# Kernel optimization log

Hardware: AMD Instinct MI355X
Metric: run time of the kernel (lower is better)

## Reference

```python
import jax, jax.numpy as jnp
import numpy as np

B, S, D, E = 4, 4096, 1024, 8
TOP_K = 2


def setup_inputs() -> dict:
    key = jax.random.key(0)
    k_x, k_gw, k_gb, k_ew, k_eb = jax.random.split(key, 5)
    x = jax.random.normal(k_x, (B, S, D), dtype=jnp.float32)
    gate_w = jax.random.normal(k_gw, (E, D), dtype=jnp.float32) * 0.02
    gate_b = jax.random.normal(k_gb, (E,), dtype=jnp.float32) * 0.02
    expert_w = jax.random.normal(k_ew, (E, D, D), dtype=jnp.float32) * 0.02
    expert_b = jax.random.normal(k_eb, (E, D), dtype=jnp.float32) * 0.02
    return {"x": x, "gate_w": gate_w, "gate_b": gate_b,
            "expert_w": expert_w, "expert_b": expert_b}


def reference(x, gate_w, gate_b, expert_w, expert_b):
    b, s, d = x.shape
    h = x.reshape(-1, d)                                  # [T, D]
    # router: linear -> softmax (fp32) -> top-k -> renormalize
    router_logits = h @ gate_w.T + gate_b                 # [T, E]
    probs = jax.nn.softmax(router_logits.astype(jnp.float32), axis=-1)
    topw, sel = jax.lax.top_k(probs, TOP_K)               # [T, K]
    topw = topw / jnp.sum(topw, axis=-1, keepdims=True)
    topw = topw.astype(h.dtype)
    out = jnp.zeros_like(h)
    for e in range(E):  # small fixed loop over experts
        # per-token combine weight for expert e (0 if not selected)
        we = jnp.sum(jnp.where(sel == e, topw, 0.0), axis=-1)  # [T]
        out = out + (h @ expert_w[e].T + expert_b[e]) * we[:, None]
    return out.reshape(b, s, d), router_logits
```

## Files before the change

kernel.cpp:

```cpp
#include <hip/hip_runtime.h>
#include <hip/hip_bf16.h>

typedef unsigned short u16;
typedef unsigned int u32;

#define T_TOK 16384
#define DIM   1024
#define NEXP  8

#define XB_OFF      0
#define WB_OFF      33554432
#define CNT_OFF     50331648
#define LIST_OFF    50332160
#define SELW_OFF    50856448
#define CONTRIB_OFF 51380736
#define WS_NEED     118489600ULL

__device__ __forceinline__ u16 f2bf(float f) {
    u32 u = __float_as_uint(f);
    u += 0x7fff + ((u >> 16) & 1);
    return (u16)(u >> 16);
}
__device__ __forceinline__ float bf2f(u16 u) {
    return __uint_as_float(((u32)u) << 16);
}

#define RT_PB 32

__global__ __launch_bounds__(256) void k_router(
    const float* __restrict__ x, const float* __restrict__ gw,
    const float* __restrict__ gb, float* __restrict__ logits,
    u16* __restrict__ xb, int* __restrict__ counts,
    int* __restrict__ lists, float4* __restrict__ selw,
    const float* __restrict__ ew, u16* __restrict__ wb)
{
    const int tid  = threadIdx.x;
    const int lane = tid & 63;
    const int w    = tid >> 6;

    __shared__ int   s_sel0[RT_PB], s_sel1[RT_PB];
    __shared__ int   s_lcnt[NEXP], s_gbase[NEXP];

    if (tid < NEXP) s_lcnt[tid] = 0;

    for (int i = 0; i < 8; ++i) {
        const int l = w * 8 + i;
        const int t = blockIdx.x * RT_PB + l;

        const float* xr = x + (size_t)t * DIM;
        float4 xs[4];
#pragma unroll
        for (int j = 0; j < 4; ++j)
            xs[j] = *reinterpret_cast<const float4*>(xr + (j * 64 + lane) * 4);

        float acc[NEXP];
#pragma unroll
        for (int e = 0; e < NEXP; ++e) {
            const float* gr = gw + e * DIM;
            float s = 0.f;
#pragma unroll
            for (int j = 0; j < 4; ++j) {
                float4 g = *reinterpret_cast<const float4*>(gr + (j * 64 + lane) * 4);
                s += xs[j].x * g.x + xs[j].y * g.y + xs[j].z * g.z + xs[j].w * g.w;
            }
            acc[e] = s;
        }
#pragma unroll
        for (int off = 1; off < 64; off <<= 1) {
#pragma unroll
            for (int e = 0; e < NEXP; ++e) acc[e] += __shfl_xor(acc[e], off);
        }
#pragma unroll
        for (int e = 0; e < NEXP; ++e) acc[e] += gb[e];

        int i0 = 0; float v0 = acc[0];
#pragma unroll
        for (int e = 1; e < NEXP; ++e) if (acc[e] > v0) { v0 = acc[e]; i0 = e; }
        int i1 = -1; float v1 = -3.4e38f;
#pragma unroll
        for (int e = 0; e < NEXP; ++e) if (e != i0 && acc[e] > v1) { v1 = acc[e]; i1 = e; }
        float e1  = __expf(v1 - v0);
        float inv = 1.f / (1.f + e1);
        float w0 = inv, w1 = e1 * inv;

        u16* xrow = xb + (size_t)t * DIM;
#pragma unroll
        for (int j = 0; j < 4; ++j) {
            int c = (j * 64 + lane) * 4;
            float4 v = xs[j];
            ushort4 u;
            u.x = f2bf(v.x); u.y = f2bf(v.y); u.z = f2bf(v.z); u.w = f2bf(v.w);
            *reinterpret_cast<ushort4*>(xrow + c) = u;
        }
        if (lane == 0) {
            float4 lo = make_float4(acc[0], acc[1], acc[2], acc[3]);
            float4 hi = make_float4(acc[4], acc[5], acc[6], acc[7]);
            *reinterpret_cast<float4*>(logits + (size_t)t * NEXP)     = lo;
            *reinterpret_cast<float4*>(logits + (size_t)t * NEXP + 4) = hi;
            selw[t] = make_float4(__int_as_float(i0), __int_as_float(i1), w0, w1);
            s_sel0[l] = i0; s_sel1[l] = i1;
        }
    }
    __syncthreads();

    int i0 = 0, i1 = 0, r0 = 0, r1 = 0;
    if (tid < RT_PB) {
        i0 = s_sel0[tid]; i1 = s_sel1[tid];
        r0 = atomicAdd(&s_lcnt[i0], 1);
        r1 = atomicAdd(&s_lcnt[i1], 1);
    }
    __syncthreads();
    if (tid < NEXP)
        s_gbase[tid] = atomicAdd(&counts[tid * 16], s_lcnt[tid]);
    __syncthreads();
    if (tid < RT_PB) {
        int t  = blockIdx.x * RT_PB + tid;
        lists[i0 * T_TOK + s_gbase[i0] + r0] = t * 2;
        lists[i1 * T_TOK + s_gbase[i1] + r1] = t * 2 + 1;
    }

    const int n4 = NEXP * DIM * DIM / 4;
    const int stride = gridDim.x * 256;
    for (int i = blockIdx.x * 256 + tid; i < n4; i += stride) {
        float4 v = reinterpret_cast<const float4*>(ew)[i];
        ushort4 u;
        u.x = f2bf(v.x); u.y = f2bf(v.y); u.z = f2bf(v.z); u.w = f2bf(v.w);
        reinterpret_cast<ushort4*>(wb)[i] = u;
    }
}


typedef __attribute__((ext_vector_type(8))) short bf16x8;
typedef __attribute__((ext_vector_type(4))) float f32x4;

#define GLDS16(g, l) __builtin_amdgcn_global_load_lds( \
    (const __attribute__((address_space(1))) void*)(g), \
    (__attribute__((address_space(3))) void*)(l), 16, 0, 0)

#define BAR() __builtin_amdgcn_s_barrier()
#define PRIO1() __builtin_amdgcn_s_setprio(1)
#define PRIO0() __builtin_amdgcn_s_setprio(0)
#define VMW0() asm volatile("s_waitcnt vmcnt(0)" ::: "memory")
#define LGKM0() do { asm volatile("s_waitcnt lgkmcnt(0)" ::: "memory"); \
                     __builtin_amdgcn_sched_barrier(0); } while (0)

__global__ __launch_bounds__(256, 2) void k_gemm(
    const u16* __restrict__ xb, const u16* __restrict__ wb,
    const int* __restrict__ counts, const int* __restrict__ lists,
    u16* __restrict__ contrib)
{
    __shared__ char lds[65536];

    const int bid = (blockIdx.x & 7) * 1024 + (blockIdx.x >> 3);
    const int e   = bid >> 10;
    const int mt  = (bid >> 3) & 127;
    const int nt  = bid & 7;
    const int cnt = counts[e * 16];
    if (mt * 128 >= cnt) return;

    const int tid  = threadIdx.x;
    const int lane = tid & 63;
    const int wid  = tid >> 6;
    const int wm   = wid >> 1;
    const int wn   = wid & 1;
    const int listbase = e * T_TOK;

    const int l8  = lane >> 3;
    const int cgs = ((lane & 7) - l8) & 7;
    const char* xbB = (const char*)xb;
    const char* wbB = (const char*)wb;
    u32 aoff[4], boff[4];
#pragma unroll
    for (int i = 0; i < 4; ++i) {
        int r    = wid * 32 + i * 8 + l8;
        int slot = mt * 128 + r;
        int tok  = lists[listbase + (slot < cnt ? slot : cnt - 1)] >> 1;
        aoff[i]  = (u32)tok * 2048 + (u32)cgs * 16;
        boff[i]  = ((u32)e << 21) + (u32)(nt * 128 + r) * 2048 + (u32)cgs * 16;
    }

#define STAGE(b, t) do { \
    _Pragma("unroll") for (int i = 0; i < 4; ++i) \
        GLDS16(xbB + aoff[i] + (t) * 128, lds + (b) * 32768 + (wid * 4 + i) * 1024); \
    _Pragma("unroll") for (int i = 0; i < 4; ++i) \
        GLDS16(wbB + boff[i] + (t) * 128, lds + (b) * 32768 + 16384 + (wid * 4 + i) * 1024); \
} while (0)

    const int l15 = lane & 15;
    const int c0  = lane >> 4;
    const u32 ra0 = (u32)(wm * 64 + l15) * 128 + (u32)(((c0 + l15) & 7) * 16);
    const u32 ra1 = (u32)(wm * 64 + l15) * 128 + (u32)(((4 + c0 + l15) & 7) * 16);
    const u32 rb0 = 16384u + (u32)(wn * 64 + l15) * 128 + (u32)(((c0 + l15) & 7) * 16);
    const u32 rb1 = 16384u + (u32)(wn * 64 + l15) * 128 + (u32)(((4 + c0 + l15) & 7) * 16);

    bf16x8 A0[8], B0[8], A1[8], B1[8];
#define LDSET(Ad, Bd, b) do { \
    _Pragma("unroll") for (int mi = 0; mi < 4; ++mi) { \
        Ad[mi * 2 + 0] = *(const bf16x8*)(lds + (b) * 32768 + ra0 + mi * 2048); \
        Ad[mi * 2 + 1] = *(const bf16x8*)(lds + (b) * 32768 + ra1 + mi * 2048); \
    } \
    _Pragma("unroll") for (int ni = 0; ni < 4; ++ni) { \
        Bd[ni * 2 + 0] = *(const bf16x8*)(lds + (b) * 32768 + rb0 + ni * 2048); \
        Bd[ni * 2 + 1] = *(const bf16x8*)(lds + (b) * 32768 + rb1 + ni * 2048); \
    } \
} while (0)

    f32x4 acc[4][4];
#pragma unroll
    for (int mi = 0; mi < 4; ++mi)
#pragma unroll
        for (int ni = 0; ni < 4; ++ni) acc[mi][ni] = (f32x4)0.f;

#define MFMAS(As, Bs) do { \
    _Pragma("unroll") for (int kk = 0; kk < 2; ++kk) \
    _Pragma("unroll") for (int mi = 0; mi < 4; ++mi) \
    _Pragma("unroll") for (int ni = 0; ni < 4; ++ni) \
        acc[mi][ni] = __builtin_amdgcn_mfma_f32_16x16x32_bf16( \
            As[mi * 2 + kk], Bs[ni * 2 + kk], acc[mi][ni], 0, 0, 0); \
} while (0)

#define ITER(U, Ac, Bc, An, Bn) do { \
    LGKM0(); \
    if ((U) >= 1) VMW0(); \
    BAR(); \
    if ((U) <= 13) STAGE((U) & 1, (U) + 2); \
    if ((U) <= 14) LDSET(An, Bn, ((U) + 1) & 1); \
    PRIO1(); MFMAS(Ac, Bc); PRIO0(); \
} while (0)

    STAGE(0, 0); STAGE(1, 1);
    VMW0(); BAR();
    LDSET(A0, B0, 0);

#pragma unroll
    for (int h = 0; h < 8; ++h) {
        ITER(2 * h,     A0, B0, A1, B1);
        ITER(2 * h + 1, A1, B1, A0, B0);
    }

    const int rbase = c0 * 4;
    const int cbase = nt * 128 + wn * 64 + l15;
#pragma unroll
    for (int mi = 0; mi < 4; ++mi) {
#pragma unroll
        for (int r = 0; r < 4; ++r) {
            int slot = mt * 128 + wm * 64 + mi * 16 + rbase + r;
            if (slot < cnt) {
                int lv = lists[listbase + slot];
                u16* crow = contrib + (size_t)lv * DIM + cbase;
#pragma unroll
                for (int ni = 0; ni < 4; ++ni)
                    crow[ni * 16] = f2bf(acc[mi][ni][r]);
            }
        }
    }
}

__global__ __launch_bounds__(256) void k_combine(
    const u16* __restrict__ contrib, const float4* __restrict__ selw,
    const float* __restrict__ eb, float* __restrict__ out)
{
    const int lane = threadIdx.x & 63;
    const int t    = blockIdx.x * 4 + (threadIdx.x >> 6);
    float4 sw = selw[t];
    const int e0 = __float_as_int(sw.x);
    const int e1 = __float_as_int(sw.y);
    const float w0 = sw.z, w1 = sw.w;
    const u16* c0 = contrib + (size_t)(t * 2) * DIM;
    const u16* c1 = c0 + DIM;
    const float* b0 = eb + e0 * DIM;
    const float* b1 = eb + e1 * DIM;
    float* orow = out + (size_t)t * DIM;
#pragma unroll
    for (int j = 0; j < 2; ++j) {
        const int c = (j * 64 + lane) * 8;
        uint4 u0 = *reinterpret_cast<const uint4*>(c0 + c);
        uint4 u1 = *reinterpret_cast<const uint4*>(c1 + c);
        const u16* p0 = (const u16*)&u0;
        const u16* p1 = (const u16*)&u1;
#pragma unroll
        for (int h = 0; h < 2; ++h) {
            float4 bb0 = *reinterpret_cast<const float4*>(b0 + c + h * 4);
            float4 bb1 = *reinterpret_cast<const float4*>(b1 + c + h * 4);
            float4 o;
            o.x = w0 * (bf2f(p0[h*4+0]) + bb0.x) + w1 * (bf2f(p1[h*4+0]) + bb1.x);
            o.y = w0 * (bf2f(p0[h*4+1]) + bb0.y) + w1 * (bf2f(p1[h*4+1]) + bb1.y);
            o.z = w0 * (bf2f(p0[h*4+2]) + bb0.z) + w1 * (bf2f(p1[h*4+2]) + bb1.z);
            o.w = w0 * (bf2f(p0[h*4+3]) + bb0.w) + w1 * (bf2f(p1[h*4+3]) + bb1.w);
            *reinterpret_cast<float4*>(orow + c + h * 4) = o;
        }
    }
}

__global__ __launch_bounds__(256) void k_bias(
    const float4* __restrict__ selw, const float* __restrict__ eb,
    float* __restrict__ out)
{
    const int lane = threadIdx.x & 63;
    const int t    = blockIdx.x * 4 + (threadIdx.x >> 6);
    float4 sw = selw[t];
    const float* b0 = eb + __float_as_int(sw.x) * DIM;
    const float* b1 = eb + __float_as_int(sw.y) * DIM;
    float* orow = out + (size_t)t * DIM;
#pragma unroll
    for (int j = 0; j < 4; ++j) {
        int c = (j * 64 + lane) * 4;
        float4 f0 = *reinterpret_cast<const float4*>(b0 + c);
        float4 f1 = *reinterpret_cast<const float4*>(b1 + c);
        float4 o;
        o.x = sw.z * f0.x + sw.w * f1.x;
        o.y = sw.z * f0.y + sw.w * f1.y;
        o.z = sw.z * f0.z + sw.w * f1.z;
        o.w = sw.z * f0.w + sw.w * f1.w;
        *reinterpret_cast<float4*>(orow + c) = o;
    }
}

__global__ __launch_bounds__(256) void k_gemm_atomic(
    const u16* __restrict__ xb, const u16* __restrict__ wb,
    const int* __restrict__ counts, const int* __restrict__ lists,
    const float4* __restrict__ selw, float* __restrict__ out)
{
    __shared__ u16 ldsA[128 * 64];
    __shared__ u16 ldsB[128 * 64];
    const int bid = blockIdx.x;
    const int e   = bid >> 10;
    const int mt  = (bid >> 3) & 127;
    const int nt  = bid & 7;
    const int cnt = counts[e * 16];
    if (mt * 128 >= cnt) return;
    const int tid  = threadIdx.x;
    const int lane = tid & 63;
    const int wid  = tid >> 6;
    const int wr   = wid >> 1, wc = wid & 1;
    const int srow = tid >> 3;
    const int skc  = (tid & 7) * 8;
    const int listbase = e * T_TOK;
    int tokA[4];
#pragma unroll
    for (int i = 0; i < 4; ++i) {
        int slot = mt * 128 + i * 32 + srow;
        tokA[i] = lists[listbase + (slot < cnt ? slot : cnt - 1)] >> 1;
    }
    const size_t wbase = ((size_t)e << 20) + (size_t)(nt * 128) * DIM;
    f32x4 acc[4][4];
#pragma unroll
    for (int mi = 0; mi < 4; ++mi)
#pragma unroll
        for (int ni = 0; ni < 4; ++ni) acc[mi][ni] = (f32x4)0.f;
    for (int k0 = 0; k0 < DIM; k0 += 64) {
        uint4 ra[4], rb[4];
#pragma unroll
        for (int i = 0; i < 4; ++i) {
            ra[i] = *reinterpret_cast<const uint4*>(xb + (size_t)tokA[i] * DIM + k0 + skc);
            rb[i] = *reinterpret_cast<const uint4*>(wb + wbase + (size_t)(i * 32 + srow) * DIM + k0 + skc);
        }
        __syncthreads();
#pragma unroll
        for (int i = 0; i < 4; ++i) {
            *reinterpret_cast<uint4*>(ldsA + (i * 32 + srow) * 64 + skc) = ra[i];
            *reinterpret_cast<uint4*>(ldsB + (i * 32 + srow) * 64 + skc) = rb[i];
        }
        __syncthreads();
#pragma unroll
        for (int ks = 0; ks < 2; ++ks) {
            const int kof = ks * 32 + (lane >> 4) * 8;
            bf16x8 af[4], bfr[4];
#pragma unroll
            for (int mi = 0; mi < 4; ++mi)
                af[mi] = *reinterpret_cast<const bf16x8*>(ldsA + (wr * 64 + mi * 16 + (lane & 15)) * 64 + kof);
#pragma unroll
            for (int ni = 0; ni < 4; ++ni)
                bfr[ni] = *reinterpret_cast<const bf16x8*>(ldsB + (wc * 64 + ni * 16 + (lane & 15)) * 64 + kof);
#pragma unroll
            for (int mi = 0; mi < 4; ++mi)
#pragma unroll
                for (int ni = 0; ni < 4; ++ni)
                    acc[mi][ni] = __builtin_amdgcn_mfma_f32_16x16x32_bf16(af[mi], bfr[ni], acc[mi][ni], 0, 0, 0);
        }
        __syncthreads();
    }
    const int rbase = (lane >> 4) * 4;
    const int cbase = nt * 128 + wc * 64 + (lane & 15);
#pragma unroll
    for (int mi = 0; mi < 4; ++mi) {
#pragma unroll
        for (int r = 0; r < 4; ++r) {
            int slot = mt * 128 + wr * 64 + mi * 16 + rbase + r;
            if (slot < cnt) {
                int lv = lists[listbase + slot];
                int tok = lv >> 1;
                float4 sw = selw[tok];
                float wgt = (lv & 1) ? sw.w : sw.z;
                float* orow = out + (size_t)tok * DIM + cbase;
#pragma unroll
                for (int ni = 0; ni < 4; ++ni)
                    atomicAdd(orow + ni * 16, acc[mi][ni][r] * wgt);
            }
        }
    }
}

extern "C" void kernel_launch(void* const* d_in, const int* in_sizes, int n_in,
                              void* d_out, int out_size, void* d_ws, size_t ws_size,
                              hipStream_t stream) {
    const float* x  = (const float*)d_in[0];
    const float* gw = (const float*)d_in[1];
    const float* gb = (const float*)d_in[2];
    const float* ew = (const float*)d_in[3];
    const float* eb = (const float*)d_in[4];

    float* out    = (float*)d_out;
    float* logits = out + (size_t)T_TOK * DIM;

    char*   ws      = (char*)d_ws;
    u16*    xb      = (u16*)(ws + XB_OFF);
    u16*    wb      = (u16*)(ws + WB_OFF);
    int*    counts  = (int*)(ws + CNT_OFF);
    int*    lists   = (int*)(ws + LIST_OFF);
    float4* selw    = (float4*)(ws + SELW_OFF);
    u16*    contrib = (u16*)(ws + CONTRIB_OFF);

    hipMemsetAsync((void*)(ws + CNT_OFF), 0, 512, stream);
    k_router<<<T_TOK / RT_PB, 256, 0, stream>>>(x, gw, gb, logits, xb, counts,
                                                lists, selw, ew, wb);

    if (ws_size >= WS_NEED) {
        k_gemm<<<NEXP * 128 * 8, 256, 0, stream>>>(xb, wb, counts, lists, contrib);
        k_combine<<<T_TOK / 4, 256, 0, stream>>>(contrib, selw, eb, out);
    } else {
        k_bias<<<T_TOK / 4, 256, 0, stream>>>(selw, eb, out);
        k_gemm_atomic<<<NEXP * 128 * 8, 256, 0, stream>>>(xb, wb, counts, lists, selw, out);
    }
}
```

Baseline: 154.7 us.

## Enlarge grouped expert GEMM tile to 256x256 with 8 waves and K=32 steps

The expert GEMM moves from 128x128 tiles with 4 waves and a K-step of 64 to 256x256 tiles with 8 waves (512 threads) and a K-step of 32. Each wave now computes a 64x128 sub-tile with 32 accumulators. The LDS swizzle and staging are redone for 64-byte rows, and the grid shrinks accordingly. The aim is more operand reuse per loaded byte and fewer blocks. The costs are higher register pressure (launch bounds 512,2), twice as many barriers per K, and coarser padding waste on the ragged per-expert token counts.

```diff
diff --git a/kernel.cpp b/kernel.cpp
--- a/kernel.cpp
+++ b/kernel.cpp
@@ -144,19 +144,19 @@
 #define LGKM0() do { asm volatile("s_waitcnt lgkmcnt(0)" ::: "memory"); \
                      __builtin_amdgcn_sched_barrier(0); } while (0)
 
-__global__ __launch_bounds__(256, 2) void k_gemm(
+__global__ __launch_bounds__(512, 2) void k_gemm(
     const u16* __restrict__ xb, const u16* __restrict__ wb,
     const int* __restrict__ counts, const int* __restrict__ lists,
     u16* __restrict__ contrib)
 {
     __shared__ char lds[65536];
 
-    const int bid = (blockIdx.x & 7) * 1024 + (blockIdx.x >> 3);
-    const int e   = bid >> 10;
-    const int mt  = (bid >> 3) & 127;
-    const int nt  = bid & 7;
+    const int bid = (blockIdx.x & 7) * 256 + (blockIdx.x >> 3);
+    const int e   = bid >> 8;
+    const int mt  = (bid >> 2) & 63;
+    const int nt  = bid & 3;
     const int cnt = counts[e * 16];
-    if (mt * 128 >= cnt) return;
+    if (mt * 256 >= cnt) return;
 
     const int tid  = threadIdx.x;
     const int lane = tid & 63;
@@ -165,66 +165,59 @@
     const int wn   = wid & 1;
     const int listbase = e * T_TOK;
 
-    const int l8  = lane >> 3;
-    const int cgs = ((lane & 7) - l8) & 7;
+    const int lr  = tid >> 2;
+    const int cgs = (((tid & 3) - lr - (lr >> 2)) & 3);
     const char* xbB = (const char*)xb;
     const char* wbB = (const char*)wb;
-    u32 aoff[4], boff[4];
-#pragma unroll
-    for (int i = 0; i < 4; ++i) {
-        int r    = wid * 32 + i * 8 + l8;
-        int slot = mt * 128 + r;
+    u32 aoff[2], boff[2];
+#pragma unroll
+    for (int i = 0; i < 2; ++i) {
+        int slot = mt * 256 + i * 128 + lr;
         int tok  = lists[listbase + (slot < cnt ? slot : cnt - 1)] >> 1;
         aoff[i]  = (u32)tok * 2048 + (u32)cgs * 16;
-        boff[i]  = ((u32)e << 21) + (u32)(nt * 128 + r) * 2048 + (u32)cgs * 16;
+        boff[i]  = ((u32)e << 21) + (u32)(nt * 256 + i * 128 + lr) * 2048 + (u32)cgs * 16;
     }
 
 #define STAGE(b, t) do { \
-    _Pragma("unroll") for (int i = 0; i < 4; ++i) \
-        GLDS16(xbB + aoff[i] + (t) * 128, lds + (b) * 32768 + (wid * 4 + i) * 1024); \
-    _Pragma("unroll") for (int i = 0; i < 4; ++i) \
-        GLDS16(wbB + boff[i] + (t) * 128, lds + (b) * 32768 + 16384 + (wid * 4 + i) * 1024); \
+    GLDS16(xbB + aoff[0] + (t) * 64, lds + (b) * 32768 + tid * 16); \
+    GLDS16(xbB + aoff[1] + (t) * 64, lds + (b) * 32768 + 8192 + tid * 16); \
+    GLDS16(wbB + boff[0] + (t) * 64, lds + (b) * 32768 + 16384 + tid * 16); \
+    GLDS16(wbB + boff[1] + (t) * 64, lds + (b) * 32768 + 24576 + tid * 16); \
 } while (0)
 
     const int l15 = lane & 15;
     const int c0  = lane >> 4;
-    const u32 ra0 = (u32)(wm * 64 + l15) * 128 + (u32)(((c0 + l15) & 7) * 16);
-    const u32 ra1 = (u32)(wm * 64 + l15) * 128 + (u32)(((4 + c0 + l15) & 7) * 16);
-    const u32 rb0 = 16384u + (u32)(wn * 64 + l15) * 128 + (u32)(((c0 + l15) & 7) * 16);
-    const u32 rb1 = 16384u + (u32)(wn * 64 + l15) * 128 + (u32)(((4 + c0 + l15) & 7) * 16);
-
-    bf16x8 A0[8], B0[8], A1[8], B1[8];
+    const u32 slotw = (u32)(((c0 + l15 + (l15 >> 2)) & 3) * 16);
+    const u32 raB = (u32)(wm * 64 + l15) * 64 + slotw;
+    const u32 rbB = 16384u + (u32)(wn * 128 + l15) * 64 + slotw;
+
+    bf16x8 A0[4], B0[8], A1[4], B1[8];
 #define LDSET(Ad, Bd, b) do { \
-    _Pragma("unroll") for (int mi = 0; mi < 4; ++mi) { \
-        Ad[mi * 2 + 0] = *(const bf16x8*)(lds + (b) * 32768 + ra0 + mi * 2048); \
-        Ad[mi * 2 + 1] = *(const bf16x8*)(lds + (b) * 32768 + ra1 + mi * 2048); \
-    } \
-    _Pragma("unroll") for (int ni = 0; ni < 4; ++ni) { \
-        Bd[ni * 2 + 0] = *(const bf16x8*)(lds + (b) * 32768 + rb0 + ni * 2048); \
-        Bd[ni * 2 + 1] = *(const bf16x8*)(lds + (b) * 32768 + rb1 + ni * 2048); \
-    } \
+    _Pragma("unroll") for (int mi = 0; mi < 4; ++mi) \
+        Ad[mi] = *(const bf16x8*)(lds + (b) * 32768 + raB + mi * 1024); \
+    _Pragma("unroll") for (int ni = 0; ni < 8; ++ni) \
+        Bd[ni] = *(const bf16x8*)(lds + (b) * 32768 + rbB + ni * 1024); \
 } while (0)
 
-    f32x4 acc[4][4];
+    f32x4 acc[4][8];
 #pragma unroll
     for (int mi = 0; mi < 4; ++mi)
 #pragma unroll
-        for (int ni = 0; ni < 4; ++ni) acc[mi][ni] = (f32x4)0.f;
+        for (int ni = 0; ni < 8; ++ni) acc[mi][ni] = (f32x4)0.f;
 
 #define MFMAS(As, Bs) do { \
-    _Pragma("unroll") for (int kk = 0; kk < 2; ++kk) \
     _Pragma("unroll") for (int mi = 0; mi < 4; ++mi) \
-    _Pragma("unroll") for (int ni = 0; ni < 4; ++ni) \
+    _Pragma("unroll") for (int ni = 0; ni < 8; ++ni) \
         acc[mi][ni] = __builtin_amdgcn_mfma_f32_16x16x32_bf16( \
-            As[mi * 2 + kk], Bs[ni * 2 + kk], acc[mi][ni], 0, 0, 0); \
+            As[mi], Bs[ni], acc[mi][ni], 0, 0, 0); \
 } while (0)
 
 #define ITER(U, Ac, Bc, An, Bn) do { \
     LGKM0(); \
     if ((U) >= 1) VMW0(); \
     BAR(); \
-    if ((U) <= 13) STAGE((U) & 1, (U) + 2); \
-    if ((U) <= 14) LDSET(An, Bn, ((U) + 1) & 1); \
+    if ((U) <= 29) STAGE((U) & 1, (U) + 2); \
+    if ((U) <= 30) LDSET(An, Bn, ((U) + 1) & 1); \
     PRIO1(); MFMAS(Ac, Bc); PRIO0(); \
 } while (0)
 
@@ -233,23 +226,23 @@
     LDSET(A0, B0, 0);
 
 #pragma unroll
-    for (int h = 0; h < 8; ++h) {
+    for (int h = 0; h < 16; ++h) {
         ITER(2 * h,     A0, B0, A1, B1);
         ITER(2 * h + 1, A1, B1, A0, B0);
     }
 
     const int rbase = c0 * 4;
-    const int cbase = nt * 128 + wn * 64 + l15;
+    const int cbase = nt * 256 + wn * 128 + l15;
 #pragma unroll
     for (int mi = 0; mi < 4; ++mi) {
 #pragma unroll
         for (int r = 0; r < 4; ++r) {
-            int slot = mt * 128 + wm * 64 + mi * 16 + rbase + r;
+            int slot = mt * 256 + wm * 64 + mi * 16 + rbase + r;
             if (slot < cnt) {
                 int lv = lists[listbase + slot];
                 u16* crow = contrib + (size_t)lv * DIM + cbase;
 #pragma unroll
-                for (int ni = 0; ni < 4; ++ni)
+                for (int ni = 0; ni < 8; ++ni)
                     crow[ni * 16] = f2bf(acc[mi][ni][r]);
             }
         }
@@ -426,7 +419,7 @@
                                                 lists, selw, ew, wb);
 
     if (ws_size >= WS_NEED) {
-        k_gemm<<<NEXP * 128 * 8, 256, 0, stream>>>(xb, wb, counts, lists, contrib);
+        k_gemm<<<NEXP * 64 * 4, 512, 0, stream>>>(xb, wb, counts, lists, contrib);
         k_combine<<<T_TOK / 4, 256, 0, stream>>>(contrib, selw, eb, out);
     } else {
         k_bias<<<T_TOK / 4, 256, 0, stream>>>(selw, eb, out);
```

Result: slower. 169.1 us (+9.3%).

## Make expert GEMM persistent with cross-tile prefetch of next M tile

Applied to the files above, without the earlier changes.

Replaces the 8192-block grid, where most blocks exit early, with 512 persistent blocks that each loop over M tiles of a fixed expert and N tile in strides of 8. The first K stages of the next tile are prefetched during the tail of the current tile, so tile turnover overlaps with compute. This removes the cost of launching and retiring empty blocks and the per-tile pipeline warmup. In exchange, load balance now depends on the expert token counts, since a block serving a busy expert runs many more iterations.

```diff
diff --git a/kernel.cpp b/kernel.cpp
--- a/kernel.cpp
+++ b/kernel.cpp
@@ -151,12 +151,11 @@
 {
     __shared__ char lds[65536];
 
-    const int bid = (blockIdx.x & 7) * 1024 + (blockIdx.x >> 3);
-    const int e   = bid >> 10;
-    const int mt  = (bid >> 3) & 127;
-    const int nt  = bid & 7;
+    const int e  = blockIdx.x & 7;
+    const int nt = (blockIdx.x >> 3) & 7;
+    const int mb = blockIdx.x >> 6;
     const int cnt = counts[e * 16];
-    if (mt * 128 >= cnt) return;
+    if (mb * 128 >= cnt) return;
 
     const int tid  = threadIdx.x;
     const int lane = tid & 63;
@@ -169,21 +168,27 @@
     const int cgs = ((lane & 7) - l8) & 7;
     const char* xbB = (const char*)xb;
     const char* wbB = (const char*)wb;
-    u32 aoff[4], boff[4];
+
+    u32 boff[4];
 #pragma unroll
     for (int i = 0; i < 4; ++i) {
-        int r    = wid * 32 + i * 8 + l8;
-        int slot = mt * 128 + r;
-        int tok  = lists[listbase + (slot < cnt ? slot : cnt - 1)] >> 1;
-        aoff[i]  = (u32)tok * 2048 + (u32)cgs * 16;
-        boff[i]  = ((u32)e << 21) + (u32)(nt * 128 + r) * 2048 + (u32)cgs * 16;
-    }
-
-#define STAGE(b, t) do { \
+        int r = wid * 32 + i * 8 + l8;
+        boff[i] = ((u32)e << 21) + (u32)(nt * 128 + r) * 2048 + (u32)cgs * 16;
+    }
+
+#define LOAD_AOFF(dst, MT) do { \
+    _Pragma("unroll") for (int i = 0; i < 4; ++i) { \
+        int r    = wid * 32 + i * 8 + l8; \
+        int slot = (MT) * 128 + r; \
+        int tok  = lists[listbase + (slot < cnt ? slot : cnt - 1)] >> 1; \
+        dst[i]   = (u32)tok * 2048 + (u32)cgs * 16; \
+    } } while (0)
+
+#define STAGE_T(b, kk, AO) do { \
     _Pragma("unroll") for (int i = 0; i < 4; ++i) \
-        GLDS16(xbB + aoff[i] + (t) * 128, lds + (b) * 32768 + (wid * 4 + i) * 1024); \
+        GLDS16(xbB + AO[i] + (kk) * 128, lds + (b) * 32768 + (wid * 4 + i) * 1024); \
     _Pragma("unroll") for (int i = 0; i < 4; ++i) \
-        GLDS16(wbB + boff[i] + (t) * 128, lds + (b) * 32768 + 16384 + (wid * 4 + i) * 1024); \
+        GLDS16(wbB + boff[i] + (kk) * 128, lds + (b) * 32768 + 16384 + (wid * 4 + i) * 1024); \
 } while (0)
 
     const int l15 = lane & 15;
@@ -219,40 +224,68 @@
             As[mi * 2 + kk], Bs[ni * 2 + kk], acc[mi][ni], 0, 0, 0); \
 } while (0)
 
-#define ITER(U, Ac, Bc, An, Bn) do { \
-    LGKM0(); \
-    if ((U) >= 1) VMW0(); \
-    BAR(); \
-    if ((U) <= 13) STAGE((U) & 1, (U) + 2); \
-    if ((U) <= 14) LDSET(An, Bn, ((U) + 1) & 1); \
-    PRIO1(); MFMAS(Ac, Bc); PRIO0(); \
-} while (0)
-
-    STAGE(0, 0); STAGE(1, 1);
+    int mtCur = mb;
+    u32 aoffA[4], aoffN[4];
+    LOAD_AOFF(aoffA, mtCur);
+
+    STAGE_T(0, 0, aoffA); STAGE_T(1, 1, aoffA);
     VMW0(); BAR();
     LDSET(A0, B0, 0);
 
-#pragma unroll
-    for (int h = 0; h < 8; ++h) {
-        ITER(2 * h,     A0, B0, A1, B1);
-        ITER(2 * h + 1, A1, B1, A0, B0);
-    }
-
-    const int rbase = c0 * 4;
-    const int cbase = nt * 128 + wn * 64 + l15;
-#pragma unroll
-    for (int mi = 0; mi < 4; ++mi) {
-#pragma unroll
-        for (int r = 0; r < 4; ++r) {
-            int slot = mt * 128 + wm * 64 + mi * 16 + rbase + r;
-            if (slot < cnt) {
-                int lv = lists[listbase + slot];
-                u16* crow = contrib + (size_t)lv * DIM + cbase;
-#pragma unroll
-                for (int ni = 0; ni < 4; ++ni)
-                    crow[ni * 16] = f2bf(acc[mi][ni][r]);
+    bool first = true;
+    while (true) {
+        const int  mtNext  = mtCur + 8;
+        const bool hasNext = mtNext * 128 < cnt;
+        if (hasNext) LOAD_AOFF(aoffN, mtNext);
+
+#pragma unroll
+        for (int u = 0; u < 16; ++u) {
+            LGKM0();
+            if (!first || u > 0) VMW0();
+            BAR();
+            if (u <= 13) {
+                STAGE_T(u & 1, u + 2, aoffA);
+            } else if (hasNext) {
+                STAGE_T(u & 1, u - 14, aoffN);
             }
-        }
+            if (u < 15) {
+                if ((u & 1) == 0) LDSET(A1, B1, 1); else LDSET(A0, B0, 0);
+            } else if (hasNext) {
+                LDSET(A0, B0, 0);
+            }
+            PRIO1();
+            if ((u & 1) == 0) MFMAS(A0, B0); else MFMAS(A1, B1);
+            PRIO0();
+        }
+
+        {
+            const int rbase = c0 * 4;
+            const int cbase = nt * 128 + wn * 64 + l15;
+#pragma unroll
+            for (int mi = 0; mi < 4; ++mi) {
+#pragma unroll
+                for (int r = 0; r < 4; ++r) {
+                    int slot = mtCur * 128 + wm * 64 + mi * 16 + rbase + r;
+                    if (slot < cnt) {
+                        int lv = lists[listbase + slot];
+                        u16* crow = contrib + (size_t)lv * DIM + cbase;
+#pragma unroll
+                        for (int ni = 0; ni < 4; ++ni)
+                            crow[ni * 16] = f2bf(acc[mi][ni][r]);
+                    }
+                }
+            }
+        }
+
+        if (!hasNext) break;
+        first = false;
+        mtCur = mtNext;
+#pragma unroll
+        for (int i = 0; i < 4; ++i) aoffA[i] = aoffN[i];
+#pragma unroll
+        for (int mi = 0; mi < 4; ++mi)
+#pragma unroll
+            for (int ni = 0; ni < 4; ++ni) acc[mi][ni] = (f32x4)0.f;
     }
 }
 
@@ -426,7 +459,7 @@
                                                 lists, selw, ew, wb);
 
     if (ws_size >= WS_NEED) {
-        k_gemm<<<NEXP * 128 * 8, 256, 0, stream>>>(xb, wb, counts, lists, contrib);
+        k_gemm<<<512, 256, 0, stream>>>(xb, wb, counts, lists, contrib);
         k_combine<<<T_TOK / 4, 256, 0, stream>>>(contrib, selw, eb, out);
     } else {
         k_bias<<<T_TOK / 4, 256, 0, stream>>>(selw, eb, out);
```

Result: slower. 239.4 us (+54.7%).
